# Optimization experiments

Hardware: AMD Instinct MI355X
Metric: run time of the kernel (lower is better)

The kernel has to match this reference:

```python
import jax, jax.numpy as jnp
import numpy as np

GAMMA = 1.0   # soft-min temperature of the differentiable DP
BIG = 1e9     # stand-in for +inf (keeps vjp NaN-free; underflows to 0 weight in softmin)


def setup_inputs() -> dict:
    key = jax.random.key(0)
    # batched pairwise cost matrix for the alignment DP
    input_array = jax.random.uniform(key, (512, 256, 256), dtype=jnp.float32)
    return {"input_array": input_array}


def reference(input_array):
    """Soft-min alignment DP (edit-distance/soft-DTW style), antidiagonal wavefront.

    D[i,j] = C[i,j] + softmin_gamma(D[i-1,j], D[i,j-1], D[i-1,j-1]); returns D[S-1,S-1].
    Diagonal k holds cells (i, j=k-i); carry = last two diagonals.
    """
    B, S, _ = input_array.shape
    i = jnp.arange(S)
    k = jnp.arange(2 * S - 1)
    js = k[:, None] - i[None, :]                 # [2S-1, S] column index j = k - i
    valid = (js >= 0) & (js < S)                 # which lanes of each diagonal exist
    js_c = jnp.clip(js, 0, S - 1)

    # pack cost diagonals: cd[k, b, i] = C[b, i, k-i]   -> [2S-1, B, S]
    cd = input_array[:, i[None, :], js_c]        # [B, 2S-1, S]
    cd = jnp.transpose(cd, (1, 0, 2))

    d0 = jnp.where(i == 0, cd[0], BIG)           # diagonal k=0: only cell (0,0)
    dm1 = jnp.full((B, S), BIG, input_array.dtype)

    def softmin(stk):                            # stk: [3, B, S]
        return -GAMMA * jax.nn.logsumexp(-stk / GAMMA, axis=0)

    def shift(d):                                # index i -> i-1, pad with BIG
        return jnp.concatenate([jnp.full((B, 1), BIG, d.dtype), d[:, :-1]], axis=1)

    def step(carry, xs):
        d1, d2 = carry                           # diagonals k-1, k-2
        c_k, v_k = xs
        # predecessors of (i, k-i): (i,j-1)->d1[i], (i-1,j)->d1[i-1], (i-1,j-1)->d2[i-1]
        preds = jnp.stack([d1, shift(d1), shift(d2)])
        d = c_k + softmin(preds)
        d = jnp.where(v_k[None, :], d, BIG)
        return (d, d1), None

    (d_last, _), _ = jax.lax.scan(step, (d0, dm1), (cd[1:], valid[1:]))
    return d_last[:, S - 1]                      # D[S-1, S-1] per batch -> [B]
```

## Files before the change

kernel.cpp:

```cpp
#include <hip/hip_runtime.h>

#define S 256
#define L2E 1.44269504088896340736f
#define LN2 0.69314718055994530942f

#define EXP2F(x) __builtin_amdgcn_exp2f(x)
#define LOG2F(x) __builtin_amdgcn_logf(x)


template <int I> __device__ __forceinline__ float comp(const float4& v) {
    if constexpr (I == 0) return v.x;
    else if constexpr (I == 1) return v.y;
    else if constexpr (I == 2) return v.z;
    else return v.w;
}

__device__ __forceinline__ float4 g4f(const float4& v) {
    float4 r;
    r.x = EXP2F(v.x * -L2E); r.y = EXP2F(v.y * -L2E);
    r.z = EXP2F(v.z * -L2E); r.w = EXP2F(v.w * -L2E);
    return r;
}

template <int P, int SB>
__device__ __forceinline__ void stepf(
    int kk, int t, int t4, const float* __restrict__ Cb,
    int rb0, int rb1, int rb2, int rb3,
    float4& c0, float4& c1, float4& c2, float4& c3,
    float4& n0, float4& n1, float4& n2, float4& n3,
    float4& xa0, float4& xa1, float4& xa2, float4& xa3,
    float4& xb0, float4& xb1, float4& xb2, float4& xb3,
    float& w10, float& w11, float& w12, float& w13,
    float& w20, float& w21, float& w22, float& w23,
    float& pd1, float& pd2)
{
    const int colr = kk + (12 - P) - t4;
    const int col  = colr < 0 ? 0 : (colr > 252 ? 252 : colr);
    const int rb   = (P == 0) ? rb0 : (P == 1) ? rb1 : (P == 2) ? rb2 : rb3;
    const float4 ld = *(const float4*)(Cb + rb + col);

    float4& cP = (P == 0) ? c0 : (P == 1) ? c1 : (P == 2) ? c2 : c3;
    float4& nP = (P == 0) ? n0 : (P == 1) ? n1 : (P == 2) ? n2 : n3;
    float4& sP = SB ? ((P == 0) ? xb0 : (P == 1) ? xb1 : (P == 2) ? xb2 : xb3)
                    : ((P == 0) ? xa0 : (P == 1) ? xa1 : (P == 2) ? xa2 : xa3);

    const bool junk = (colr > 260);
    float4 gq;
    gq.x = junk ? 0.0f : EXP2F(sP.x * -L2E);
    gq.y = junk ? 0.0f : EXP2F(sP.y * -L2E);
    gq.z = junk ? 0.0f : EXP2F(sP.z * -L2E);
    gq.w = junk ? 0.0f : EXP2F(sP.w * -L2E);
    cP = nP;
    nP = gq;
    sP = ld;

    const float g0 = comp<(P    ) & 3>(c0);
    const float g1 = comp<(P + 3) & 3>(c1);
    const float g2 = comp<(P + 2) & 3>(c2);
    const float g3 = comp<(P + 1) & 3>(c3);

    const float e0 = g0 * (w10 + pd1 + pd2);
    const float e1 = g1 * (w11 + w10 + w20);
    const float e2 = g2 * (w12 + w11 + w21);
    const float e3 = g3 * (w13 + w12 + w22);

    w20 = w10; w21 = w11; w22 = w12; w23 = w13;
    w10 = e0;  w11 = e1;  w12 = e2;  w13 = e3;

    const float nx = __shfl_up(e3, 1);
    pd2 = pd1;
    pd1 = (t == 0) ? 0.0f : nx;
}

__global__ __launch_bounds__(64, 1) void dp_softmin_wave(const float* __restrict__ C,
                                                         float* __restrict__ out) {
    const int b = blockIdx.x;
    const int t = threadIdx.x;
    const float* Cb = C + ((size_t)b << 16);
    const int t4 = 4 * t;

    const int rb0 = (t4 + 0) << 8;
    const int rb1 = (t4 + 1) << 8;
    const int rb2 = (t4 + 2) << 8;
    const int rb3 = (t4 + 3) << 8;

    auto cl = [](int c) { return c < 0 ? 0 : (c > 252 ? 252 : c); };
    auto q  = [&](int rb, int col) { return *(const float4*)(Cb + rb + col); };

    float4 c0 = g4f(q(rb0, 0)), c1 = g4f(q(rb1, 0)),
           c2 = g4f(q(rb2, 0)), c3 = g4f(q(rb3, 0));
    float4 n0 = g4f(q(rb0, cl(4 - t4)));
    float4 n1 = c1, n2 = c2, n3 = c3;
    float4 xa0 = q(rb0, cl(12 - t4));
    float4 xa1 = q(rb1, cl(4 - t4));
    float4 xa2 = q(rb2, cl(4 - t4));
    float4 xa3 = q(rb3, cl(4 - t4));
    float4 xb0 = q(rb0, cl(8 - t4));
    float4 xb1 = q(rb1, cl(8 - t4));
    float4 xb2 = q(rb2, cl(8 - t4));
    float4 xb3 = q(rb3, cl(8 - t4));

    float w10 = 0.0f, w11 = 0.0f, w12 = 0.0f, w13 = 0.0f;
    float w20 = 0.0f, w21 = 0.0f, w22 = 0.0f, w23 = 0.0f;
    float pd1 = 0.0f, pd2 = 0.0f;
    int sig = 0;

    if (t == 0) w10 = c0.x;

#define ARGS t, t4, Cb, rb0, rb1, rb2, rb3, c0,c1,c2,c3, n0,n1,n2,n3, \
             xa0,xa1,xa2,xa3, xb0,xb1,xb2,xb3, \
             w10,w11,w12,w13, w20,w21,w22,w23, pd1,pd2

    stepf<1,0>(1, ARGS);
    stepf<2,0>(2, ARGS);
    stepf<3,0>(3, ARGS);
    stepf<0,1>(4, ARGS);
    stepf<1,1>(5, ARGS);
    stepf<2,1>(6, ARGS);
    stepf<3,1>(7, ARGS);

#pragma clang loop unroll(disable)
    for (int kb = 8; kb <= 496; kb += 8) {
        if ((kb & 63) == 0) {
            float M = fmaxf(fmaxf(fmaxf(w10, w11), fmaxf(w12, w13)),
                            fmaxf(fmaxf(w20, w21), fmaxf(w22, w23)));
            #pragma unroll
            for (int m = 1; m < 64; m <<= 1) M = fmaxf(M, __shfl_xor(M, m));
            int e = ((__float_as_int(M) >> 23) & 255) - 127;
            float f = __int_as_float((127 - e) << 23);
            w10 *= f; w11 *= f; w12 *= f; w13 *= f;
            w20 *= f; w21 *= f; w22 *= f; w23 *= f;
            pd1 *= f; pd2 *= f;
            sig -= e;
        }
        stepf<0,0>(kb + 0, ARGS);
        stepf<1,0>(kb + 1, ARGS);
        stepf<2,0>(kb + 2, ARGS);
        stepf<3,0>(kb + 3, ARGS);
        stepf<0,1>(kb + 4, ARGS);
        stepf<1,1>(kb + 5, ARGS);
        stepf<2,1>(kb + 6, ARGS);
        stepf<3,1>(kb + 7, ARGS);
    }

    stepf<0,0>(504, ARGS);
    stepf<1,0>(505, ARGS);
    stepf<2,0>(506, ARGS);
    stepf<3,0>(507, ARGS);
    stepf<0,1>(508, ARGS);
    stepf<1,1>(509, ARGS);
    stepf<2,1>(510, ARGS);
#undef ARGS

    if (t == 63) out[b] = ((float)sig - LOG2F(w13)) * LN2;
}

extern "C" void kernel_launch(void* const* d_in, const int* in_sizes, int n_in,
                              void* d_out, int out_size, void* d_ws, size_t ws_size,
                              hipStream_t stream) {
    const float* C = (const float*)d_in[0];
    float* out = (float*)d_out;
    dp_softmin_wave<<<512, 64, 0, stream>>>(C, out);
}
```

Before: 75.56 us.

## Interleave two independent batch DPs per wavefront to hide latency

Each 64-thread block now processes two batch elements (b and b+256) with fully duplicated register state, interleaving their wavefront steps, and the grid shrinks from 512 to 256 blocks. The two independent dependency chains give the scheduler instruction-level parallelism to hide exp/shuffle/load latency within one wave. In exchange it doubles register pressure and halves the number of blocks. With 256 blocks on a GPU of roughly that many CUs, per-CU concurrency may fall, and serial work per wave doubles.

```diff
diff --git a/kernel.cpp b/kernel.cpp
--- a/kernel.cpp
+++ b/kernel.cpp
@@ -1,6 +1,5 @@
 #include <hip/hip_runtime.h>
 
-#define S 256
 #define L2E 1.44269504088896340736f
 #define LN2 0.69314718055994530942f
 
@@ -76,7 +75,8 @@
                                                          float* __restrict__ out) {
     const int b = blockIdx.x;
     const int t = threadIdx.x;
-    const float* Cb = C + ((size_t)b << 16);
+    const float* CbA = C + ((size_t)b << 16);
+    const float* CbB = C + (((size_t)b + 256) << 16);
     const int t4 = 4 * t;
 
     const int rb0 = (t4 + 0) << 8;
@@ -85,74 +85,93 @@
     const int rb3 = (t4 + 3) << 8;
 
     auto cl = [](int c) { return c < 0 ? 0 : (c > 252 ? 252 : c); };
-    auto q  = [&](int rb, int col) { return *(const float4*)(Cb + rb + col); };
+    auto q4 = [](const float* base, int rb, int col) {
+        return *(const float4*)(base + rb + col);
+    };
 
-    float4 c0 = g4f(q(rb0, 0)), c1 = g4f(q(rb1, 0)),
-           c2 = g4f(q(rb2, 0)), c3 = g4f(q(rb3, 0));
-    float4 n0 = g4f(q(rb0, cl(4 - t4)));
-    float4 n1 = c1, n2 = c2, n3 = c3;
-    float4 xa0 = q(rb0, cl(12 - t4));
-    float4 xa1 = q(rb1, cl(4 - t4));
-    float4 xa2 = q(rb2, cl(4 - t4));
-    float4 xa3 = q(rb3, cl(4 - t4));
-    float4 xb0 = q(rb0, cl(8 - t4));
-    float4 xb1 = q(rb1, cl(8 - t4));
-    float4 xb2 = q(rb2, cl(8 - t4));
-    float4 xb3 = q(rb3, cl(8 - t4));
+    float4 Ac0 = g4f(q4(CbA, rb0, 0)), Ac1 = g4f(q4(CbA, rb1, 0)),
+           Ac2 = g4f(q4(CbA, rb2, 0)), Ac3 = g4f(q4(CbA, rb3, 0));
+    float4 An0 = g4f(q4(CbA, rb0, cl(4 - t4)));
+    float4 An1 = Ac1, An2 = Ac2, An3 = Ac3;
+    float4 Axa0 = q4(CbA, rb0, cl(12 - t4));
+    float4 Axa1 = q4(CbA, rb1, cl(4 - t4));
+    float4 Axa2 = q4(CbA, rb2, cl(4 - t4));
+    float4 Axa3 = q4(CbA, rb3, cl(4 - t4));
+    float4 Axb0 = q4(CbA, rb0, cl(8 - t4)), Axb1 = q4(CbA, rb1, cl(8 - t4));
+    float4 Axb2 = q4(CbA, rb2, cl(8 - t4)), Axb3 = q4(CbA, rb3, cl(8 - t4));
+    float Aw10 = 0.0f, Aw11 = 0.0f, Aw12 = 0.0f, Aw13 = 0.0f;
+    float Aw20 = 0.0f, Aw21 = 0.0f, Aw22 = 0.0f, Aw23 = 0.0f;
+    float Apd1 = 0.0f, Apd2 = 0.0f;
+    int sigA = 0;
+    if (t == 0) Aw10 = Ac0.x;
 
-    float w10 = 0.0f, w11 = 0.0f, w12 = 0.0f, w13 = 0.0f;
-    float w20 = 0.0f, w21 = 0.0f, w22 = 0.0f, w23 = 0.0f;
-    float pd1 = 0.0f, pd2 = 0.0f;
-    int sig = 0;
+    float4 Bc0 = g4f(q4(CbB, rb0, 0)), Bc1 = g4f(q4(CbB, rb1, 0)),
+           Bc2 = g4f(q4(CbB, rb2, 0)), Bc3 = g4f(q4(CbB, rb3, 0));
+    float4 Bn0 = g4f(q4(CbB, rb0, cl(4 - t4)));
+    float4 Bn1 = Bc1, Bn2 = Bc2, Bn3 = Bc3;
+    float4 Bxa0 = q4(CbB, rb0, cl(12 - t4));
+    float4 Bxa1 = q4(CbB, rb1, cl(4 - t4));
+    float4 Bxa2 = q4(CbB, rb2, cl(4 - t4));
+    float4 Bxa3 = q4(CbB, rb3, cl(4 - t4));
+    float4 Bxb0 = q4(CbB, rb0, cl(8 - t4)), Bxb1 = q4(CbB, rb1, cl(8 - t4));
+    float4 Bxb2 = q4(CbB, rb2, cl(8 - t4)), Bxb3 = q4(CbB, rb3, cl(8 - t4));
+    float Bw10 = 0.0f, Bw11 = 0.0f, Bw12 = 0.0f, Bw13 = 0.0f;
+    float Bw20 = 0.0f, Bw21 = 0.0f, Bw22 = 0.0f, Bw23 = 0.0f;
+    float Bpd1 = 0.0f, Bpd2 = 0.0f;
+    int sigB = 0;
+    if (t == 0) Bw10 = Bc0.x;
 
-    if (t == 0) w10 = c0.x;
+#define ARGS_A t, t4, CbA, rb0, rb1, rb2, rb3, Ac0,Ac1,Ac2,Ac3, An0,An1,An2,An3, \
+               Axa0,Axa1,Axa2,Axa3, Axb0,Axb1,Axb2,Axb3, \
+               Aw10,Aw11,Aw12,Aw13, Aw20,Aw21,Aw22,Aw23, Apd1,Apd2
+#define ARGS_B t, t4, CbB, rb0, rb1, rb2, rb3, Bc0,Bc1,Bc2,Bc3, Bn0,Bn1,Bn2,Bn3, \
+               Bxa0,Bxa1,Bxa2,Bxa3, Bxb0,Bxb1,Bxb2,Bxb3, \
+               Bw10,Bw11,Bw12,Bw13, Bw20,Bw21,Bw22,Bw23, Bpd1,Bpd2
+#define STEP2(kk, P, SB) do { stepf<P,SB>(kk, ARGS_A); stepf<P,SB>(kk, ARGS_B); } while (0)
 
-#define ARGS t, t4, Cb, rb0, rb1, rb2, rb3, c0,c1,c2,c3, n0,n1,n2,n3, \
-             xa0,xa1,xa2,xa3, xb0,xb1,xb2,xb3, \
-             w10,w11,w12,w13, w20,w21,w22,w23, pd1,pd2
-
-    stepf<1,0>(1, ARGS);
-    stepf<2,0>(2, ARGS);
-    stepf<3,0>(3, ARGS);
-    stepf<0,1>(4, ARGS);
-    stepf<1,1>(5, ARGS);
-    stepf<2,1>(6, ARGS);
-    stepf<3,1>(7, ARGS);
+    STEP2(1, 1, 0); STEP2(2, 2, 0); STEP2(3, 3, 0);
+    STEP2(4, 0, 1); STEP2(5, 1, 1); STEP2(6, 2, 1); STEP2(7, 3, 1);
 
 #pragma clang loop unroll(disable)
     for (int kb = 8; kb <= 496; kb += 8) {
         if ((kb & 63) == 0) {
-            float M = fmaxf(fmaxf(fmaxf(w10, w11), fmaxf(w12, w13)),
-                            fmaxf(fmaxf(w20, w21), fmaxf(w22, w23)));
+            float MA = fmaxf(fmaxf(fmaxf(Aw10, Aw11), fmaxf(Aw12, Aw13)),
+                             fmaxf(fmaxf(Aw20, Aw21), fmaxf(Aw22, Aw23)));
+            float MB = fmaxf(fmaxf(fmaxf(Bw10, Bw11), fmaxf(Bw12, Bw13)),
+                             fmaxf(fmaxf(Bw20, Bw21), fmaxf(Bw22, Bw23)));
             #pragma unroll
-            for (int m = 1; m < 64; m <<= 1) M = fmaxf(M, __shfl_xor(M, m));
-            int e = ((__float_as_int(M) >> 23) & 255) - 127;
-            float f = __int_as_float((127 - e) << 23);
-            w10 *= f; w11 *= f; w12 *= f; w13 *= f;
-            w20 *= f; w21 *= f; w22 *= f; w23 *= f;
-            pd1 *= f; pd2 *= f;
-            sig -= e;
+            for (int m = 1; m < 64; m <<= 1) {
+                MA = fmaxf(MA, __shfl_xor(MA, m));
+                MB = fmaxf(MB, __shfl_xor(MB, m));
+            }
+            int eA = ((__float_as_int(MA) >> 23) & 255) - 127;
+            int eB = ((__float_as_int(MB) >> 23) & 255) - 127;
+            float fA = __int_as_float((127 - eA) << 23);
+            float fB = __int_as_float((127 - eB) << 23);
+            Aw10 *= fA; Aw11 *= fA; Aw12 *= fA; Aw13 *= fA;
+            Aw20 *= fA; Aw21 *= fA; Aw22 *= fA; Aw23 *= fA;
+            Apd1 *= fA; Apd2 *= fA; sigA -= eA;
+            Bw10 *= fB; Bw11 *= fB; Bw12 *= fB; Bw13 *= fB;
+            Bw20 *= fB; Bw21 *= fB; Bw22 *= fB; Bw23 *= fB;
+            Bpd1 *= fB; Bpd2 *= fB; sigB -= eB;
         }
-        stepf<0,0>(kb + 0, ARGS);
-        stepf<1,0>(kb + 1, ARGS);
-        stepf<2,0>(kb + 2, ARGS);
-        stepf<3,0>(kb + 3, ARGS);
-        stepf<0,1>(kb + 4, ARGS);
-        stepf<1,1>(kb + 5, ARGS);
-        stepf<2,1>(kb + 6, ARGS);
-        stepf<3,1>(kb + 7, ARGS);
+        STEP2(kb + 0, 0, 0); STEP2(kb + 1, 1, 0);
+        STEP2(kb + 2, 2, 0); STEP2(kb + 3, 3, 0);
+        STEP2(kb + 4, 0, 1); STEP2(kb + 5, 1, 1);
+        STEP2(kb + 6, 2, 1); STEP2(kb + 7, 3, 1);
     }
 
-    stepf<0,0>(504, ARGS);
-    stepf<1,0>(505, ARGS);
-    stepf<2,0>(506, ARGS);
-    stepf<3,0>(507, ARGS);
-    stepf<0,1>(508, ARGS);
-    stepf<1,1>(509, ARGS);
-    stepf<2,1>(510, ARGS);
-#undef ARGS
+    STEP2(504, 0, 0); STEP2(505, 1, 0); STEP2(506, 2, 0); STEP2(507, 3, 0);
+    STEP2(508, 0, 1); STEP2(509, 1, 1); STEP2(510, 2, 1);
 
-    if (t == 63) out[b] = ((float)sig - LOG2F(w13)) * LN2;
+#undef STEP2
+#undef ARGS_A
+#undef ARGS_B
+
+    if (t == 63) {
+        out[b]       = ((float)sigA - LOG2F(Aw13)) * LN2;
+        out[b + 256] = ((float)sigB - LOG2F(Bw13)) * LN2;
+    }
 }
 
 extern "C" void kernel_launch(void* const* d_in, const int* in_sizes, int n_in,
@@ -160,5 +179,5 @@
                               hipStream_t stream) {
     const float* C = (const float*)d_in[0];
     float* out = (float*)d_out;
-    dp_softmin_wave<<<512, 64, 0, stream>>>(C, out);
+    dp_softmin_wave<<<256, 64, 0, stream>>>(C, out);
 }
```

Result: slower. 133.3 us (+76.4%).
